# Kernel optimization log

Measured on AMD Instinct MI355X. Metric: run time of the kernel, lower is better.

The kernel has to match this reference:

```python
import jax, jax.numpy as jnp
import numpy as np

OUT, IN, BLK = 11008, 4096, 128

def setup_inputs() -> dict:
    key = jax.random.key(0)
    k1, k2, k3, k4, k5 = jax.random.split(key, 5)
    x = jax.random.normal(k1, (64, IN), dtype=jnp.float32)
    weight = jax.random.randint(k2, (OUT, IN // 2), 0, 256, dtype=jnp.int32)  # packed uint4 pairs
    scale = jax.random.uniform(k3, (OUT, 1, BLK), dtype=jnp.float32) * 0.01 + 1e-4
    zp = jax.random.randint(k4, (OUT, 1, BLK), 0, 16).astype(jnp.float32)
    bias = jax.random.normal(k5, (OUT,), dtype=jnp.float32)
    return {"x": x, "weight": weight, "scale": scale, "zp": zp, "bias": bias}

def reference(x, weight, scale, zp, bias):
    dtype = x.dtype
    # unpack: high nibble first, then low nibble (interleaved along in_features)
    w_h = (weight >> 4) & 15
    w_l = weight & 15
    w_unpacked = jnp.stack((w_h, w_l), axis=-1).reshape(OUT, IN)
    # block-wise dequant: scale/zp shaped [OUT, 1, BLK], broadcast over block index dim
    w_blocked = w_unpacked.reshape(OUT, IN // BLK, BLK).astype(dtype)
    w_rec = ((w_blocked - zp.astype(dtype)) * scale.astype(dtype)).reshape(OUT, IN)
    return x @ w_rec.T + bias
```

## Files before the change

### kernel.cpp

```cpp
#include <hip/hip_runtime.h>

#define OUT_F 11008
#define IN_F  4096
#define PKW   2048
#define BLKQ  128

typedef __attribute__((ext_vector_type(8))) short          s16x8;
typedef __attribute__((ext_vector_type(8))) unsigned short u16x8;
typedef __attribute__((ext_vector_type(4))) float          f32x4;
typedef __attribute__((ext_vector_type(4))) int            i32x4;

__device__ __forceinline__ unsigned short f2bf(float f) {
    union { float f; unsigned u; } v; v.f = f;
    unsigned r = v.u + 0x8000u + ((v.u >> 16) & 1u);
    return (unsigned short)(r >> 16);
}

__global__ void prep_xfrag(const float* __restrict__ x, unsigned short* __restrict__ xf) {
    int kb   = blockIdx.x;
    int t    = threadIdx.x;
    int mt   = t >> 6;
    int lane = t & 63;
    int m  = mt * 16 + (lane & 15);
    int k0 = kb * 32 + (lane >> 4) * 8;
    const float* xp = x + m * IN_F + k0;
    f32x4 a = *(const f32x4*)(xp);
    f32x4 b = *(const f32x4*)(xp + 4);
    u16x8 v;
    v[0] = f2bf(a[0]); v[1] = f2bf(a[1]); v[2] = f2bf(a[2]); v[3] = f2bf(a[3]);
    v[4] = f2bf(b[0]); v[5] = f2bf(b[1]); v[6] = f2bf(b[2]); v[7] = f2bf(b[3]);
    *(u16x8*)(xf + (size_t)((kb * 4 + mt) * 64 + lane) * 8) = v;
}

__global__ __launch_bounds__(256) void qlin_main(
    const int*   __restrict__ wq,
    const float* __restrict__ scale,
    const float* __restrict__ zp,
    const float* __restrict__ bias,
    const unsigned short* __restrict__ xf,
    float* __restrict__ out)
{
    __shared__ __align__(16) float lf[4096];

    const int t      = threadIdx.x;
    const int o_base = blockIdx.x * 16;
    const int wave   = t >> 6;
    const int lane   = t & 63;
    const int col16  = lane & 15;
    const int quad   = lane >> 4;
    const int row    = o_base + col16;

    float s[32];
    unsigned zpn[4];
    {
        const float* sp  = scale + (size_t)row * BLKQ;
        const float* zpp = zp    + (size_t)row * BLKQ;
        #pragma unroll
        for (int p = 0; p < 4; ++p) {
            int off = p * 32 + quad * 8;
            f32x4 s0 = *(const f32x4*)(sp + off);
            f32x4 s1 = *(const f32x4*)(sp + off + 4);
            f32x4 z0 = *(const f32x4*)(zpp + off);
            f32x4 z1 = *(const f32x4*)(zpp + off + 4);
            unsigned pk = 0;
            #pragma unroll
            for (int c = 0; c < 4; ++c) {
                s[p * 8 + c]     = s0[c];
                s[p * 8 + 4 + c] = s1[c];
                pk |= ((unsigned)z0[c]) << (4 * c);
                pk |= ((unsigned)z1[c]) << (4 * (c + 4));
            }
            zpn[p] = pk;
        }
    }

    const int* wp = wq + (size_t)row * PKW + wave * 512 + quad * 4;
    const s16x8* xfv = (const s16x8*)xf;
    const int kgb = wave * 32;

    f32x4 acc[4];
    #pragma unroll
    for (int mt = 0; mt < 4; ++mt) acc[mt] = (f32x4){0.f, 0.f, 0.f, 0.f};

    i32x4 wr[4];
    #pragma unroll
    for (int p = 0; p < 4; ++p) wr[p] = *(const i32x4*)(wp + p * 16);

    s16x8 ar[2][4];
    #pragma unroll
    for (int sl = 0; sl < 2; ++sl)
        #pragma unroll
        for (int mt = 0; mt < 4; ++mt)
            ar[sl][mt] = xfv[(size_t)(((kgb + sl) * 4 + mt) * 64 + lane)];

    for (int kb4 = 0; kb4 < 8; ++kb4) {
        #pragma unroll
        for (int p = 0; p < 4; ++p) {
            const int kb = kb4 * 4 + p;

            int kn = kb + 4; if (kn > 31) kn = 31;
            i32x4 wnext = *(const i32x4*)(wp + kn * 16);

            u16x8 ub;
            #pragma unroll
            for (int e = 0; e < 8; ++e) {
                unsigned dw = (unsigned)wr[p][e >> 1];
                int wi = (e & 1) ? (int)(dw & 15u) : (int)((dw >> 4) & 15u);
                int zi = (int)((zpn[p] >> (4 * e)) & 15u);
                ub[e] = f2bf((float)(wi - zi) * s[p * 8 + e]);
            }
            s16x8 bfrag;
            #pragma unroll
            for (int e = 0; e < 8; ++e) bfrag[e] = (short)ub[e];

            #pragma unroll
            for (int mt = 0; mt < 4; ++mt)
                acc[mt] = __builtin_amdgcn_mfma_f32_16x16x32_bf16(ar[p & 1][mt], bfrag, acc[mt], 0, 0, 0);

            int ka = kb + 2; if (ka > 31) ka = 31;
            #pragma unroll
            for (int mt = 0; mt < 4; ++mt)
                ar[p & 1][mt] = xfv[(size_t)(((kgb + ka) * 4 + mt) * 64 + lane)];

            wr[p] = wnext;
        }
    }

    #pragma unroll
    for (int mt = 0; mt < 4; ++mt) {
        #pragma unroll
        for (int r = 0; r < 4; ++r) {
            int m = mt * 16 + quad * 4 + r;
            lf[wave * 1024 + m * 16 + col16] = acc[mt][r];
        }
    }
    __syncthreads();
    #pragma unroll
    for (int p = 0; p < 4; ++p) {
        int e = p * 256 + t;
        int m = e >> 4, col = e & 15;
        float v = lf[e] + lf[1024 + e] + lf[2048 + e] + lf[3072 + e] + bias[o_base + col];
        out[(size_t)m * OUT_F + o_base + col] = v;
    }
}

extern "C" void kernel_launch(void* const* d_in, const int* in_sizes, int n_in,
                              void* d_out, int out_size, void* d_ws, size_t ws_size,
                              hipStream_t stream) {
    const float* x     = (const float*)d_in[0];
    const int*   wq    = (const int*)d_in[1];
    const float* scale = (const float*)d_in[2];
    const float* zpv   = (const float*)d_in[3];
    const float* bias  = (const float*)d_in[4];
    float* out = (float*)d_out;
    unsigned short* xf = (unsigned short*)d_ws;

    prep_xfrag<<<128, 256, 0, stream>>>(x, xf);
    qlin_main<<<OUT_F / 16, 256, 0, stream>>>(wq, scale, zpv, bias, xf, out);
}
```

Baseline: 165.8 us.

## Split K across four blocks per output tile with atomic accumulation

Each 16-row output tile is now handled by four blocks, each covering a quarter of the input dimension. That gives four times as many workgroups to fill the GPU, and each wave keeps a single scale/zero-point slice and preloads all of its weight fragments up front. Partial sums are combined with float atomicAdd into an output that a new kernel first fills with the bias. The cost is an extra init kernel, atomic traffic to global memory, and float summation order that is no longer deterministic.

```diff
diff --git a/kernel.cpp b/kernel.cpp
--- a/kernel.cpp
+++ b/kernel.cpp
@@ -14,6 +14,11 @@
     union { float f; unsigned u; } v; v.f = f;
     unsigned r = v.u + 0x8000u + ((v.u >> 16) & 1u);
     return (unsigned short)(r >> 16);
+}
+
+__global__ void init_out(const float* __restrict__ bias, float* __restrict__ out) {
+    int idx = blockIdx.x * 256 + threadIdx.x;
+    out[idx] = bias[idx % OUT_F];
 }
 
 __global__ void prep_xfrag(const float* __restrict__ x, unsigned short* __restrict__ xf) {
@@ -36,93 +41,82 @@
     const int*   __restrict__ wq,
     const float* __restrict__ scale,
     const float* __restrict__ zp,
-    const float* __restrict__ bias,
     const unsigned short* __restrict__ xf,
     float* __restrict__ out)
 {
     __shared__ __align__(16) float lf[4096];
 
     const int t      = threadIdx.x;
-    const int o_base = blockIdx.x * 16;
+    const int oi     = blockIdx.x >> 2;
+    const int kc     = blockIdx.x & 3;
+    const int o_base = oi * 16;
     const int wave   = t >> 6;
     const int lane   = t & 63;
     const int col16  = lane & 15;
     const int quad   = lane >> 4;
     const int row    = o_base + col16;
 
-    float s[32];
-    unsigned zpn[4];
+    float s[8];
+    unsigned zpn;
     {
-        const float* sp  = scale + (size_t)row * BLKQ;
-        const float* zpp = zp    + (size_t)row * BLKQ;
+        const float* sp  = scale + (size_t)row * BLKQ + wave * 32 + quad * 8;
+        const float* zpp = zp    + (size_t)row * BLKQ + wave * 32 + quad * 8;
+        f32x4 s0 = *(const f32x4*)(sp);
+        f32x4 s1 = *(const f32x4*)(sp + 4);
+        f32x4 z0 = *(const f32x4*)(zpp);
+        f32x4 z1 = *(const f32x4*)(zpp + 4);
+        unsigned pk = 0;
         #pragma unroll
-        for (int p = 0; p < 4; ++p) {
-            int off = p * 32 + quad * 8;
-            f32x4 s0 = *(const f32x4*)(sp + off);
-            f32x4 s1 = *(const f32x4*)(sp + off + 4);
-            f32x4 z0 = *(const f32x4*)(zpp + off);
-            f32x4 z1 = *(const f32x4*)(zpp + off + 4);
-            unsigned pk = 0;
-            #pragma unroll
-            for (int c = 0; c < 4; ++c) {
-                s[p * 8 + c]     = s0[c];
-                s[p * 8 + 4 + c] = s1[c];
-                pk |= ((unsigned)z0[c]) << (4 * c);
-                pk |= ((unsigned)z1[c]) << (4 * (c + 4));
-            }
-            zpn[p] = pk;
+        for (int c = 0; c < 4; ++c) {
+            s[c]     = s0[c];
+            s[4 + c] = s1[c];
+            pk |= ((unsigned)z0[c]) << (4 * c);
+            pk |= ((unsigned)z1[c]) << (4 * (c + 4));
         }
+        zpn = pk;
     }
 
-    const int* wp = wq + (size_t)row * PKW + wave * 512 + quad * 4;
+    const int* wp = wq + (size_t)row * PKW + kc * 512 + wave * 16 + quad * 4;
     const s16x8* xfv = (const s16x8*)xf;
-    const int kgb = wave * 32;
+    const int kgb0 = kc * 32 + wave;
 
-    f32x4 acc[4];
+    i32x4 wr[8];
     #pragma unroll
-    for (int mt = 0; mt < 4; ++mt) acc[mt] = (f32x4){0.f, 0.f, 0.f, 0.f};
-
-    i32x4 wr[4];
-    #pragma unroll
-    for (int p = 0; p < 4; ++p) wr[p] = *(const i32x4*)(wp + p * 16);
+    for (int j = 0; j < 8; ++j) wr[j] = *(const i32x4*)(wp + j * 64);
 
     s16x8 ar[2][4];
     #pragma unroll
     for (int sl = 0; sl < 2; ++sl)
         #pragma unroll
         for (int mt = 0; mt < 4; ++mt)
-            ar[sl][mt] = xfv[(size_t)(((kgb + sl) * 4 + mt) * 64 + lane)];
+            ar[sl][mt] = xfv[(size_t)(((kgb0 + 4 * sl) * 4 + mt) * 64 + lane)];
 
-    for (int kb4 = 0; kb4 < 8; ++kb4) {
+    f32x4 acc[4];
+    #pragma unroll
+    for (int mt = 0; mt < 4; ++mt) acc[mt] = (f32x4){0.f, 0.f, 0.f, 0.f};
+
+    #pragma unroll
+    for (int j = 0; j < 8; ++j) {
+        u16x8 ub;
         #pragma unroll
-        for (int p = 0; p < 4; ++p) {
-            const int kb = kb4 * 4 + p;
+        for (int e = 0; e < 8; ++e) {
+            unsigned dw = (unsigned)wr[j][e >> 1];
+            int wi = (e & 1) ? (int)(dw & 15u) : (int)((dw >> 4) & 15u);
+            int zi = (int)((zpn >> (4 * e)) & 15u);
+            ub[e] = f2bf((float)(wi - zi) * s[e]);
+        }
+        s16x8 bfrag;
+        #pragma unroll
+        for (int e = 0; e < 8; ++e) bfrag[e] = (short)ub[e];
 
-            int kn = kb + 4; if (kn > 31) kn = 31;
-            i32x4 wnext = *(const i32x4*)(wp + kn * 16);
+        #pragma unroll
+        for (int mt = 0; mt < 4; ++mt)
+            acc[mt] = __builtin_amdgcn_mfma_f32_16x16x32_bf16(ar[j & 1][mt], bfrag, acc[mt], 0, 0, 0);
 
-            u16x8 ub;
-            #pragma unroll
-            for (int e = 0; e < 8; ++e) {
-                unsigned dw = (unsigned)wr[p][e >> 1];
-                int wi = (e & 1) ? (int)(dw & 15u) : (int)((dw >> 4) & 15u);
-                int zi = (int)((zpn[p] >> (4 * e)) & 15u);
-                ub[e] = f2bf((float)(wi - zi) * s[p * 8 + e]);
-            }
-            s16x8 bfrag;
-            #pragma unroll
-            for (int e = 0; e < 8; ++e) bfrag[e] = (short)ub[e];
-
+        if (j < 6) {
             #pragma unroll
             for (int mt = 0; mt < 4; ++mt)
-                acc[mt] = __builtin_amdgcn_mfma_f32_16x16x32_bf16(ar[p & 1][mt], bfrag, acc[mt], 0, 0, 0);
-
-            int ka = kb + 2; if (ka > 31) ka = 31;
-            #pragma unroll
-            for (int mt = 0; mt < 4; ++mt)
-                ar[p & 1][mt] = xfv[(size_t)(((kgb + ka) * 4 + mt) * 64 + lane)];
-
-            wr[p] = wnext;
+                ar[j & 1][mt] = xfv[(size_t)(((kgb0 + 4 * (j + 2)) * 4 + mt) * 64 + lane)];
         }
     }
 
@@ -139,8 +133,8 @@
     for (int p = 0; p < 4; ++p) {
         int e = p * 256 + t;
         int m = e >> 4, col = e & 15;
-        float v = lf[e] + lf[1024 + e] + lf[2048 + e] + lf[3072 + e] + bias[o_base + col];
-        out[(size_t)m * OUT_F + o_base + col] = v;
+        float v = lf[e] + lf[1024 + e] + lf[2048 + e] + lf[3072 + e];
+        atomicAdd(&out[(size_t)m * OUT_F + o_base + col], v);
     }
 }
 
@@ -155,6 +149,7 @@
     float* out = (float*)d_out;
     unsigned short* xf = (unsigned short*)d_ws;
 
+    init_out<<<(64 * OUT_F) / 256, 256, 0, stream>>>(bias, out);
     prep_xfrag<<<128, 256, 0, stream>>>(x, xf);
-    qlin_main<<<OUT_F / 16, 256, 0, stream>>>(wq, scale, zpv, bias, xf, out);
+    qlin_main<<<(OUT_F / 16) * 4, 256, 0, stream>>>(wq, scale, zpv, xf, out);
 }
```

Measured after the change: 172.0 us. +3.7%, slower.
